# Kernel optimization log

Measured on AMD Instinct MI355X. Metric: run time of the kernel, lower is better.

The kernel has to match this reference:

```python
import jax, jax.numpy as jnp
import numpy as np

IN_DIM = 512

def setup_inputs() -> dict:
    key = jax.random.key(0)
    ks = jax.random.split(key, 7)
    s = 1.0 / np.sqrt(IN_DIM)
    x = jax.random.normal(ks[0], (8, 2048, IN_DIM), dtype=jnp.float32)
    Wq = jax.random.uniform(ks[1], (IN_DIM, IN_DIM), jnp.float32, -s, s)
    bq = jax.random.uniform(ks[2], (IN_DIM,), jnp.float32, -s, s)
    Wk = jax.random.uniform(ks[3], (IN_DIM, IN_DIM), jnp.float32, -s, s)
    bk = jax.random.uniform(ks[4], (IN_DIM,), jnp.float32, -s, s)
    Wv = jax.random.uniform(ks[5], (IN_DIM, IN_DIM), jnp.float32, -s, s)
    bv = jax.random.uniform(ks[6], (IN_DIM,), jnp.float32, -s, s)
    return {"x": x, "Wq": Wq, "bq": bq, "Wk": Wk, "bk": bk, "Wv": Wv, "bv": bv}

def reference(x, Wq, bq, Wk, bk, Wv, bv):
    # Q,K,V projections: torch Linear is x @ W.T + b; Wq here is [out,in]
    q = jnp.einsum('bsc,dc->bsd', x, Wq) + bq
    k = jnp.einsum('bsc,dc->bsd', x, Wk) + bk
    v = jnp.einsum('bsc,dc->bsd', x, Wv) + bv
    energy = jnp.einsum('bqd,bkd->bqk', q, k)  # no scaling, matches source
    attention = jax.nn.softmax(energy, axis=-1)
    out = jnp.einsum('bqk,bkd->bqd', attention, v)
    return out
```

## Files before the change

### kernel.cpp

```cpp
#include <hip/hip_runtime.h>

typedef unsigned short u16;
typedef _Float16 f16;

using half8   = __attribute__((ext_vector_type(8))) _Float16;
using f32x4   = __attribute__((ext_vector_type(4))) float;
using ushort8 = __attribute__((ext_vector_type(8))) unsigned short;
using us4     = __attribute__((ext_vector_type(4))) unsigned short;
using float4v = __attribute__((ext_vector_type(4))) float;

#define B_  8
#define S_  2048
#define D_  512
#define BK  32
#define TILE_ELEMS 4096
#define BUF_ELEMS  8192

__device__ __forceinline__ u16 f2h(float f) {
  f16 h = (f16)f;
  u16 u;
  __builtin_memcpy(&u, &h, 2);
  return u;
}

__device__ __forceinline__ float h2f(u16 h) {
  f16 x;
  __builtin_memcpy(&x, &h, 2);
  return (float)x;
}

__device__ __forceinline__ void stage16(const void* g, void* l) {
  __builtin_amdgcn_global_load_lds((const __attribute__((address_space(1))) void*)g,
                                   (__attribute__((address_space(3))) void*)l,
                                   16, 0, 0);
}

__device__ __forceinline__ void xcd_remap(int& bx, int& by, int& bz) {
  const int lin = ((int)blockIdx.z * (int)gridDim.y + (int)blockIdx.y) * (int)gridDim.x
                  + (int)blockIdx.x;
  const int nwg = (int)gridDim.x * (int)gridDim.y * (int)gridDim.z;
  const int swz = (lin & 7) * (nwg >> 3) + (lin >> 3);
  bx = swz % (int)gridDim.x;
  const int tmp = swz / (int)gridDim.x;
  by = tmp % (int)gridDim.y;
  bz = tmp / (int)gridDim.y;
}

__device__ __forceinline__ void gemm_core(const u16* __restrict__ A, const u16* __restrict__ B,
                                          int K, int m0, int n0,
                                          u16* lds, f32x4 acc[4][4]) {
  const int tid  = threadIdx.x;
  const int lane = tid & 63;
  const int wave = tid >> 6;
  const int wr = wave >> 1, wc = wave & 1;
  const int fr   = lane & 15;
  const int fgrp = lane >> 4;

  int sr[2], sc[2];
  #pragma unroll
  for (int s = 0; s < 2; ++s) {
    const int p    = tid * 16 + s * 4096;
    const int R    = p >> 7;
    const int slot = (p >> 4) & 7;
    const int s0   = slot ^ (R & 7);
    sr[s] = 2 * R + (s0 >> 2);
    sc[s] = (s0 & 3) * 8;
  }

  int offA[4], offB[4];
  #pragma unroll
  for (int m = 0; m < 4; ++m) {
    const int ra = wr * 64 + m * 16 + fr;
    const int Ra = ra >> 1;
    offA[m] = Ra * 128 + (((((ra & 1) << 2) | fgrp) ^ (Ra & 7)) << 4);
    const int rb = wc * 64 + m * 16 + fr;
    const int Rb = rb >> 1;
    offB[m] = Rb * 128 + (((((rb & 1) << 2) | fgrp) ^ (Rb & 7)) << 4);
  }

  const f32x4 vzero = {0.f, 0.f, 0.f, 0.f};
  #pragma unroll
  for (int m = 0; m < 4; ++m)
    #pragma unroll
    for (int n = 0; n < 4; ++n)
      acc[m][n] = vzero;

  const int T = K / BK;

  auto STAGE = [&](int t, u16* buf) {
    #pragma unroll
    for (int s = 0; s < 2; ++s) {
      stage16(A + (size_t)(m0 + sr[s]) * K + t * BK + sc[s],
              buf + s * 2048 + wave * 512);
      stage16(B + (size_t)(n0 + sr[s]) * K + t * BK + sc[s],
              buf + TILE_ELEMS + s * 2048 + wave * 512);
    }
  };

  STAGE(0, lds);
  STAGE(1, lds + BUF_ELEMS);

  int r = 0;
  for (int u = 0; u < T; ++u) {
    if (u + 1 < T) {
      asm volatile("s_waitcnt vmcnt(4)\n\ts_barrier" ::: "memory");
    } else {
      asm volatile("s_waitcnt vmcnt(0)\n\ts_barrier" ::: "memory");
    }
    const u16* buf = lds + r * BUF_ELEMS;
    half8 a[4], b[4];
    #pragma unroll
    for (int m = 0; m < 4; ++m)
      a[m] = *(const half8*)((const char*)buf + offA[m]);
    #pragma unroll
    for (int n = 0; n < 4; ++n)
      b[n] = *(const half8*)((const char*)(buf + TILE_ELEMS) + offB[n]);
    if (u + 2 < T)
      STAGE(u + 2, lds + (r == 0 ? 2 : r - 1) * BUF_ELEMS);
    __builtin_amdgcn_s_setprio(1);
    #pragma unroll
    for (int m = 0; m < 4; ++m)
      #pragma unroll
      for (int n = 0; n < 4; ++n)
        acc[m][n] = __builtin_amdgcn_mfma_f32_16x16x32_f16(a[m], b[n], acc[m][n], 0, 0, 0);
    __builtin_amdgcn_s_setprio(0);
    r = (r == 2) ? 0 : r + 1;
  }
}

__global__ __launch_bounds__(256) void proj_kernel(
    const u16* __restrict__ xh, const u16* __restrict__ Wh,
    const float* __restrict__ bq, const float* __restrict__ bk, const float* __restrict__ bv,
    u16* __restrict__ Qb, u16* __restrict__ Kb, u16* __restrict__ Vt) {
  __shared__ __align__(16) u16 lds[3 * BUF_ELEMS];
  int bx, by, bz;
  xcd_remap(bx, by, bz);
  const int z  = bz;
  const int m0 = by * 128;
  const int n0 = bx * 128;
  const u16* W = Wh + (size_t)z * D_ * D_;
  const float* bias = (z == 0) ? bq : (z == 1) ? bk : bv;
  f32x4 acc[4][4];
  gemm_core(xh, W, D_, m0, n0, lds, acc);

  const int lane = threadIdx.x & 63;
  const int wave = threadIdx.x >> 6;
  const int wr = wave >> 1, wc = wave & 1;
  #pragma unroll
  for (int m = 0; m < 4; ++m) {
    const int gr0 = m0 + wr * 64 + m * 16 + ((lane >> 4) << 2);
    #pragma unroll
    for (int n = 0; n < 4; ++n) {
      const int gc = n0 + wc * 64 + n * 16 + (lane & 15);
      const float bb = bias[gc];
      if (z < 2) {
        u16* O = z ? Kb : Qb;
        #pragma unroll
        for (int r = 0; r < 4; ++r)
          O[(size_t)(gr0 + r) * D_ + gc] = f2h(acc[m][n][r] + bb);
      } else {
        const int bidx = gr0 >> 11;
        const int s    = gr0 & 2047;
        us4 p;
        #pragma unroll
        for (int r = 0; r < 4; ++r) p[r] = f2h(acc[m][n][r] + bb);
        *(us4*)(Vt + ((size_t)bidx * D_ + gc) * S_ + s) = p;
      }
    }
  }
}

__global__ __launch_bounds__(256) void qk_kernel(
    const u16* __restrict__ Qb, const u16* __restrict__ Kb, u16* __restrict__ E,
    size_t sA, size_t sE) {
  __shared__ __align__(16) u16 lds[3 * BUF_ELEMS];
  int bx, by, bz;
  xcd_remap(bx, by, bz);
  const int z  = bz;
  const int m0 = by * 128;
  const int n0 = bx * 128;
  f32x4 acc[4][4];
  gemm_core(Qb + (size_t)z * sA, Kb + (size_t)z * sA, D_, m0, n0, lds, acc);

  u16* Eb = E + (size_t)z * sE;
  const int lane = threadIdx.x & 63;
  const int wave = threadIdx.x >> 6;
  const int wr = wave >> 1, wc = wave & 1;
  #pragma unroll
  for (int m = 0; m < 4; ++m) {
    const int gr0 = m0 + wr * 64 + m * 16 + ((lane >> 4) << 2);
    #pragma unroll
    for (int n = 0; n < 4; ++n) {
      const int gc = n0 + wc * 64 + n * 16 + (lane & 15);
      #pragma unroll
      for (int r = 0; r < 4; ++r)
        Eb[(size_t)(gr0 + r) * S_ + gc] = f2h(acc[m][n][r]);
    }
  }
}

__global__ __launch_bounds__(256) void softmax_kernel(u16* __restrict__ E) {
  const int row  = blockIdx.x * 4 + (threadIdx.x >> 6);
  const int lane = threadIdx.x & 63;
  u16* R = E + (size_t)row * S_;
  float e[32];
  #pragma unroll
  for (int i = 0; i < 4; ++i) {
    ushort8 v = *(const ushort8*)(R + i * 512 + lane * 8);
    #pragma unroll
    for (int j = 0; j < 8; ++j) e[i * 8 + j] = h2f(v[j]);
  }
  float m = e[0];
  #pragma unroll
  for (int i = 1; i < 32; ++i) m = fmaxf(m, e[i]);
  for (int off = 32; off > 0; off >>= 1) m = fmaxf(m, __shfl_xor(m, off, 64));
  float s = 0.f;
  #pragma unroll
  for (int i = 0; i < 32; ++i) { e[i] = __expf(e[i] - m); s += e[i]; }
  for (int off = 32; off > 0; off >>= 1) s += __shfl_xor(s, off, 64);
  const float inv = 1.f / s;
  #pragma unroll
  for (int i = 0; i < 4; ++i) {
    ushort8 v;
    #pragma unroll
    for (int j = 0; j < 8; ++j) v[j] = f2h(e[i * 8 + j] * inv);
    *(ushort8*)(R + i * 512 + lane * 8) = v;
  }
}

__global__ __launch_bounds__(256) void pv_kernel(
    const u16* __restrict__ P, const u16* __restrict__ Vt, float* __restrict__ out,
    size_t sP, size_t sV, size_t sO) {
  __shared__ __align__(16) u16 lds[3 * BUF_ELEMS];
  int bx, by, bz;
  xcd_remap(bx, by, bz);
  const int z  = bz;
  const int m0 = by * 128;
  const int n0 = bx * 128;
  f32x4 acc[4][4];
  gemm_core(P + (size_t)z * sP, Vt + (size_t)z * sV, S_, m0, n0, lds, acc);

  float* Ob = out + (size_t)z * sO;
  const int lane = threadIdx.x & 63;
  const int wave = threadIdx.x >> 6;
  const int wr = wave >> 1, wc = wave & 1;
  #pragma unroll
  for (int m = 0; m < 4; ++m) {
    const int gr0 = m0 + wr * 64 + m * 16 + ((lane >> 4) << 2);
    #pragma unroll
    for (int n = 0; n < 4; ++n) {
      const int gc = n0 + wc * 64 + n * 16 + (lane & 15);
      #pragma unroll
      for (int r = 0; r < 4; ++r)
        Ob[(size_t)(gr0 + r) * D_ + gc] = acc[m][n][r];
    }
  }
}

__global__ __launch_bounds__(256) void cvt_kernel(const float* __restrict__ in,
                                                  u16* __restrict__ out, int n8) {
  const int i = blockIdx.x * 256 + threadIdx.x;
  if (i >= n8) return;
  const float4v a = *(const float4v*)(in + (size_t)i * 8);
  const float4v b = *(const float4v*)(in + (size_t)i * 8 + 4);
  ushort8 o;
  o[0] = f2h(a[0]); o[1] = f2h(a[1]); o[2] = f2h(a[2]); o[3] = f2h(a[3]);
  o[4] = f2h(b[0]); o[5] = f2h(b[1]); o[6] = f2h(b[2]); o[7] = f2h(b[3]);
  *(ushort8*)(out + (size_t)i * 8) = o;
}

__global__ __launch_bounds__(256) void cvt3_kernel(const float* __restrict__ w0,
                                                   const float* __restrict__ w1,
                                                   const float* __restrict__ w2,
                                                   u16* __restrict__ out, int n8) {
  const int i = blockIdx.x * 256 + threadIdx.x;
  if (i >= n8) return;
  const float* in = (blockIdx.y == 0) ? w0 : (blockIdx.y == 1) ? w1 : w2;
  u16* o_ = out + (size_t)blockIdx.y * D_ * D_;
  const float4v a = *(const float4v*)(in + (size_t)i * 8);
  const float4v b = *(const float4v*)(in + (size_t)i * 8 + 4);
  ushort8 o;
  o[0] = f2h(a[0]); o[1] = f2h(a[1]); o[2] = f2h(a[2]); o[3] = f2h(a[3]);
  o[4] = f2h(b[0]); o[5] = f2h(b[1]); o[6] = f2h(b[2]); o[7] = f2h(b[3]);
  *(ushort8*)(o_ + (size_t)i * 8) = o;
}

extern "C" void kernel_launch(void* const* d_in, const int* in_sizes, int n_in,
                              void* d_out, int out_size, void* d_ws, size_t ws_size,
                              hipStream_t stream) {
  (void)in_sizes; (void)n_in; (void)out_size;
  const float* x  = (const float*)d_in[0];
  const float* Wq = (const float*)d_in[1];
  const float* bq = (const float*)d_in[2];
  const float* Wk = (const float*)d_in[3];
  const float* bk = (const float*)d_in[4];
  const float* Wv = (const float*)d_in[5];
  const float* bv = (const float*)d_in[6];
  float* out = (float*)d_out;

  char* ws = (char*)d_ws;
  size_t off = 0;
  auto alloc = [&](size_t bytes) -> char* {
    char* p = ws + off;
    off += (bytes + 255) & ~(size_t)255;
    return p;
  };
  const size_t MS = (size_t)B_ * S_;
  u16* xh = (u16*)alloc(MS * D_ * 2);
  u16* Wh = (u16*)alloc(3ull * D_ * D_ * 2);
  u16* Qb = (u16*)alloc(MS * D_ * 2);
  u16* Kb = (u16*)alloc(MS * D_ * 2);
  u16* Vt = (u16*)alloc(MS * D_ * 2);
  const size_t Efull = (size_t)B_ * S_ * S_ * 2;
  const bool full = ws_size >= off + Efull;
  u16* E = (u16*)alloc(full ? Efull : (size_t)S_ * S_ * 2);

  {
    const int n8 = (int)(MS * D_ / 8);
    cvt_kernel<<<dim3((n8 + 255) / 256), dim3(256), 0, stream>>>(x, xh, n8);
    const int w8 = D_ * D_ / 8;
    cvt3_kernel<<<dim3((w8 + 255) / 256, 3), dim3(256), 0, stream>>>(Wq, Wk, Wv, Wh, w8);
  }

  proj_kernel<<<dim3(D_ / 128, MS / 128, 3), dim3(256), 0, stream>>>(
      xh, Wh, bq, bk, bv, Qb, Kb, Vt);

  if (full) {
    qk_kernel<<<dim3(S_ / 128, S_ / 128, B_), dim3(256), 0, stream>>>(
        Qb, Kb, E, (size_t)S_ * D_, (size_t)S_ * S_);
    softmax_kernel<<<dim3(B_ * S_ / 4), dim3(256), 0, stream>>>(E);
    pv_kernel<<<dim3(D_ / 128, S_ / 128, B_), dim3(256), 0, stream>>>(
        E, Vt, out, (size_t)S_ * S_, (size_t)D_ * S_, (size_t)S_ * D_);
  } else {
    for (int b = 0; b < B_; ++b) {
      qk_kernel<<<dim3(S_ / 128, S_ / 128, 1), dim3(256), 0, stream>>>(
          Qb + (size_t)b * S_ * D_, Kb + (size_t)b * S_ * D_, E, 0, 0);
      softmax_kernel<<<dim3(S_ / 4), dim3(256), 0, stream>>>(E);
      pv_kernel<<<dim3(D_ / 128, S_ / 128, 1), dim3(256), 0, stream>>>(
          E, Vt + (size_t)b * D_ * S_, out + (size_t)b * S_ * D_, 0, 0, 0);
    }
  }
}
```

Before: 161.7 us.

## Warp-specialize QK and PV GEMMs with producer waves and 128x256 tiles

```diff
diff --git a/kernel.cpp b/kernel.cpp
--- a/kernel.cpp
+++ b/kernel.cpp
@@ -12,9 +12,10 @@
 #define B_  8
 #define S_  2048
 #define D_  512
-#define BK  32
-#define TILE_ELEMS 4096
-#define BUF_ELEMS  8192
+
+#define VMCNT(N)  asm volatile("s_waitcnt vmcnt(" #N ")" ::: "memory")
+#define LGKM0()   asm volatile("s_waitcnt lgkmcnt(0)" ::: "memory")
+#define SBAR()    asm volatile("s_barrier" ::: "memory")
 
 __device__ __forceinline__ u16 f2h(float f) {
   f16 h = (f16)f;
@@ -46,9 +47,11 @@
   bz = tmp / (int)gridDim.y;
 }
 
-__device__ __forceinline__ void gemm_core(const u16* __restrict__ A, const u16* __restrict__ B,
-                                          int K, int m0, int n0,
-                                          u16* lds, f32x4 acc[4][4]) {
+__device__ __forceinline__ void gemm128(const u16* __restrict__ A, const u16* __restrict__ B,
+                                        int K, int m0, int n0,
+                                        u16* lds, f32x4 acc[4][4]) {
+  constexpr int TILE_ELEMS = 4096;
+  constexpr int BUF_ELEMS  = 8192;
   const int tid  = threadIdx.x;
   const int lane = tid & 63;
   const int wave = tid >> 6;
@@ -85,14 +88,14 @@
     for (int n = 0; n < 4; ++n)
       acc[m][n] = vzero;
 
-  const int T = K / BK;
+  const int T = K / 32;
 
   auto STAGE = [&](int t, u16* buf) {
     #pragma unroll
     for (int s = 0; s < 2; ++s) {
-      stage16(A + (size_t)(m0 + sr[s]) * K + t * BK + sc[s],
+      stage16(A + (size_t)(m0 + sr[s]) * K + t * 32 + sc[s],
               buf + s * 2048 + wave * 512);
-      stage16(B + (size_t)(n0 + sr[s]) * K + t * BK + sc[s],
+      stage16(B + (size_t)(n0 + sr[s]) * K + t * 32 + sc[s],
               buf + TILE_ELEMS + s * 2048 + wave * 512);
     }
   };
@@ -128,11 +131,126 @@
   }
 }
 
+constexpr int WS_BUFE = 12288;
+constexpr int WS_ABYT = 8192;
+
+__device__ __forceinline__ void ws_producer(const u16* __restrict__ A,
+                                            const u16* __restrict__ B,
+                                            int K, int m0, int n0, u16* lds) {
+  const int lane = threadIdx.x & 63;
+  const int pw   = (threadIdx.x >> 6) - 4;
+  const u16* src[6];
+  int dstE[6];
+  #pragma unroll
+  for (int i = 0; i < 6; ++i) {
+    const int gidx = pw * 6 + i;
+    const int pt   = gidx * 1024 + lane * 16;
+    const bool isA = (pt < WS_ABYT);
+    const int q    = isA ? pt : (pt - WS_ABYT);
+    const int R    = q >> 7;
+    const int s0   = ((q >> 4) & 7) ^ (R & 7);
+    const int row  = 2 * R + (s0 >> 2);
+    const int col  = (s0 & 3) * 8;
+    src[i]  = (isA ? A + (size_t)(m0 + row) * K : B + (size_t)(n0 + row) * K) + col;
+    dstE[i] = gidx * 512;
+  }
+  const int NT = K / 32;
+  #pragma unroll
+  for (int i = 0; i < 6; ++i) stage16(src[i], lds + dstE[i]);
+  #pragma unroll
+  for (int i = 0; i < 6; ++i) stage16(src[i] + 32, lds + WS_BUFE + dstE[i]);
+  int pb = 2;
+  for (int t = 0; t < NT; ++t) {
+    if (t + 2 < NT) {
+      u16* bb = lds + pb * WS_BUFE;
+      #pragma unroll
+      for (int i = 0; i < 6; ++i) stage16(src[i] + (t + 2) * 32, bb + dstE[i]);
+      VMCNT(6);
+    } else {
+      VMCNT(0);
+    }
+    SBAR();
+    pb = (pb == 2) ? 0 : pb + 1;
+  }
+}
+
+__device__ __forceinline__ void ws_consumer(int K, const u16* lds, f32x4 acc[4][8]) {
+  const int lane = threadIdx.x & 63;
+  const int wave = threadIdx.x >> 6;
+  const int wr = wave >> 1, wc = wave & 1;
+  const int fr = lane & 15, fgrp = lane >> 4;
+
+  int offA[4], offB[8];
+  #pragma unroll
+  for (int m = 0; m < 4; ++m) {
+    const int ra = wr * 64 + m * 16 + fr;
+    const int Ra = ra >> 1;
+    offA[m] = Ra * 128 + (((((ra & 1) << 2) | fgrp) ^ (Ra & 7)) << 4);
+  }
+  #pragma unroll
+  for (int n = 0; n < 8; ++n) {
+    const int rb = wc * 128 + n * 16 + fr;
+    const int Rb = rb >> 1;
+    offB[n] = WS_ABYT + Rb * 128 + (((((rb & 1) << 2) | fgrp) ^ (Rb & 7)) << 4);
+  }
+
+  const f32x4 vzero = {0.f, 0.f, 0.f, 0.f};
+  #pragma unroll
+  for (int m = 0; m < 4; ++m)
+    #pragma unroll
+    for (int n = 0; n < 8; ++n)
+      acc[m][n] = vzero;
+
+  const int NT = K / 32;
+  half8 aE[4], bE[8], aO[4], bO[8];
+
+#define READF(BI, AA, BB)                                                        \
+  {                                                                              \
+    const char* _b = (const char*)lds + (BI) * (WS_BUFE * 2);                    \
+    _Pragma("unroll")                                                            \
+    for (int m = 0; m < 4; ++m) AA[m] = *(const half8*)(_b + offA[m]);           \
+    _Pragma("unroll")                                                            \
+    for (int n = 0; n < 8; ++n) BB[n] = *(const half8*)(_b + offB[n]);           \
+  }
+#define MFMA_T(AA, BB)                                                           \
+  __builtin_amdgcn_s_setprio(1);                                                 \
+  _Pragma("unroll")                                                              \
+  for (int m = 0; m < 4; ++m)                                                    \
+    _Pragma("unroll")                                                            \
+    for (int n = 0; n < 8; ++n)                                                  \
+      acc[m][n] = __builtin_amdgcn_mfma_f32_16x16x32_f16(AA[m], BB[n],           \
+                                                         acc[m][n], 0, 0, 0);    \
+  __builtin_amdgcn_s_setprio(0);
+
+  SBAR();
+  READF(0, aE, bE);
+  READF(1, aO, bO);
+  MFMA_T(aE, bE);
+  LGKM0();
+  int ib = 2;
+  for (int t = 1; t + 1 < NT; t += 2) {
+    SBAR();
+    READF(ib, aE, bE);
+    MFMA_T(aO, bO);
+    LGKM0();
+    SBAR();
+    const int ib2 = (ib == 2) ? 0 : ib + 1;
+    if (t + 2 < NT) READF(ib2, aO, bO);
+    MFMA_T(aE, bE);
+    LGKM0();
+    ib = (ib2 == 2) ? 0 : ib2 + 1;
+  }
+  SBAR();
+  MFMA_T(aO, bO);
+#undef READF
+#undef MFMA_T
+}
+
 __global__ __launch_bounds__(256) void proj_kernel(
     const u16* __restrict__ xh, const u16* __restrict__ Wh,
     const float* __restrict__ bq, const float* __restrict__ bk, const float* __restrict__ bv,
     u16* __restrict__ Qb, u16* __restrict__ Kb, u16* __restrict__ Vt) {
-  __shared__ __align__(16) u16 lds[3 * BUF_ELEMS];
+  __shared__ __align__(16) u16 lds[3 * 8192];
   int bx, by, bz;
   xcd_remap(bx, by, bz);
   const int z  = bz;
@@ -141,7 +259,7 @@
   const u16* W = Wh + (size_t)z * D_ * D_;
   const float* bias = (z == 0) ? bq : (z == 1) ? bk : bv;
   f32x4 acc[4][4];
-  gemm_core(xh, W, D_, m0, n0, lds, acc);
+  gemm128(xh, W, D_, m0, n0, lds, acc);
 
   const int lane = threadIdx.x & 63;
   const int wave = threadIdx.x >> 6;
@@ -170,28 +288,32 @@
   }
 }
 
-__global__ __launch_bounds__(256) void qk_kernel(
+__global__ __launch_bounds__(512, 1) void qk_kernel(
     const u16* __restrict__ Qb, const u16* __restrict__ Kb, u16* __restrict__ E,
     size_t sA, size_t sE) {
-  __shared__ __align__(16) u16 lds[3 * BUF_ELEMS];
+  __shared__ __align__(16) u16 lds[3 * WS_BUFE];
   int bx, by, bz;
   xcd_remap(bx, by, bz);
   const int z  = bz;
   const int m0 = by * 128;
-  const int n0 = bx * 128;
-  f32x4 acc[4][4];
-  gemm_core(Qb + (size_t)z * sA, Kb + (size_t)z * sA, D_, m0, n0, lds, acc);
+  const int n0 = bx * 256;
+  const u16* A = Qb + (size_t)z * sA;
+  const u16* B = Kb + (size_t)z * sA;
+  const int wave = threadIdx.x >> 6;
+  if (wave >= 4) { ws_producer(A, B, D_, m0, n0, lds); return; }
+
+  f32x4 acc[4][8];
+  ws_consumer(D_, lds, acc);
 
   u16* Eb = E + (size_t)z * sE;
   const int lane = threadIdx.x & 63;
-  const int wave = threadIdx.x >> 6;
   const int wr = wave >> 1, wc = wave & 1;
   #pragma unroll
   for (int m = 0; m < 4; ++m) {
     const int gr0 = m0 + wr * 64 + m * 16 + ((lane >> 4) << 2);
     #pragma unroll
-    for (int n = 0; n < 4; ++n) {
-      const int gc = n0 + wc * 64 + n * 16 + (lane & 15);
+    for (int n = 0; n < 8; ++n) {
+      const int gc = n0 + wc * 128 + n * 16 + (lane & 15);
       #pragma unroll
       for (int r = 0; r < 4; ++r)
         Eb[(size_t)(gr0 + r) * S_ + gc] = f2h(acc[m][n][r]);
@@ -228,28 +350,32 @@
   }
 }
 
-__global__ __launch_bounds__(256) void pv_kernel(
+__global__ __launch_bounds__(512, 1) void pv_kernel(
     const u16* __restrict__ P, const u16* __restrict__ Vt, float* __restrict__ out,
     size_t sP, size_t sV, size_t sO) {
-  __shared__ __align__(16) u16 lds[3 * BUF_ELEMS];
+  __shared__ __align__(16) u16 lds[3 * WS_BUFE];
   int bx, by, bz;
   xcd_remap(bx, by, bz);
   const int z  = bz;
   const int m0 = by * 128;
-  const int n0 = bx * 128;
-  f32x4 acc[4][4];
-  gemm_core(P + (size_t)z * sP, Vt + (size_t)z * sV, S_, m0, n0, lds, acc);
+  const int n0 = bx * 256;
+  const u16* A = P + (size_t)z * sP;
+  const u16* B = Vt + (size_t)z * sV;
+  const int wave = threadIdx.x >> 6;
+  if (wave >= 4) { ws_producer(A, B, S_, m0, n0, lds); return; }
+
+  f32x4 acc[4][8];
+  ws_consumer(S_, lds, acc);
 
   float* Ob = out + (size_t)z * sO;
   const int lane = threadIdx.x & 63;
-  const int wave = threadIdx.x >> 6;
   const int wr = wave >> 1, wc = wave & 1;
   #pragma unroll
   for (int m = 0; m < 4; ++m) {
     const int gr0 = m0 + wr * 64 + m * 16 + ((lane >> 4) << 2);
     #pragma unroll
-    for (int n = 0; n < 4; ++n) {
-      const int gc = n0 + wc * 64 + n * 16 + (lane & 15);
+    for (int n = 0; n < 8; ++n) {
+      const int gc = n0 + wc * 128 + n * 16 + (lane & 15);
       #pragma unroll
       for (int r = 0; r < 4; ++r)
         Ob[(size_t)(gr0 + r) * D_ + gc] = acc[m][n][r];
@@ -326,17 +452,17 @@
       xh, Wh, bq, bk, bv, Qb, Kb, Vt);
 
   if (full) {
-    qk_kernel<<<dim3(S_ / 128, S_ / 128, B_), dim3(256), 0, stream>>>(
+    qk_kernel<<<dim3(S_ / 256, S_ / 128, B_), dim3(512), 0, stream>>>(
         Qb, Kb, E, (size_t)S_ * D_, (size_t)S_ * S_);
     softmax_kernel<<<dim3(B_ * S_ / 4), dim3(256), 0, stream>>>(E);
-    pv_kernel<<<dim3(D_ / 128, S_ / 128, B_), dim3(256), 0, stream>>>(
+    pv_kernel<<<dim3(D_ / 256, S_ / 128, B_), dim3(512), 0, stream>>>(
         E, Vt, out, (size_t)S_ * S_, (size_t)D_ * S_, (size_t)S_ * D_);
   } else {
     for (int b = 0; b < B_; ++b) {
-      qk_kernel<<<dim3(S_ / 128, S_ / 128, 1), dim3(256), 0, stream>>>(
+      qk_kernel<<<dim3(S_ / 256, S_ / 128, 1), dim3(512), 0, stream>>>(
           Qb + (size_t)b * S_ * D_, Kb + (size_t)b * S_ * D_, E, 0, 0);
       softmax_kernel<<<dim3(S_ / 4), dim3(256), 0, stream>>>(E);
-      pv_kernel<<<dim3(D_ / 128, S_ / 128, 1), dim3(256), 0, stream>>>(
+      pv_kernel<<<dim3(D_ / 256, S_ / 128, 1), dim3(512), 0, stream>>>(
           E, Vt + (size_t)b * D_ * S_, out + (size_t)b * S_ * D_, 0, 0, 0);
     }
   }
```

New measurement: 172.5 us. +6.7%, slower.
